# Optimization experiments

Hardware: AMD Instinct MI355X
Metric: run time of the kernel (lower is better)

## Reference

```python
import jax, jax.numpy as jnp
import numpy as np
from jax import lax

DIM = 384
NE = 8
TOPK = 2
HID = 4 * DIM
N, H, W = 32, 32, 32
EPS = 1e-6


def setup_inputs() -> dict:
    key = jax.random.key(0)
    ks = jax.random.split(key, 12)
    s = 0.02
    return {
        "input": jax.random.normal(ks[0], (N, DIM, H, W), dtype=jnp.float32),
        "dw_w": jax.random.normal(ks[1], (DIM, 1, 7, 7), dtype=jnp.float32) * s,
        "dw_b": jnp.zeros((DIM,), dtype=jnp.float32),
        "ln_g": jnp.ones((DIM,), dtype=jnp.float32),
        "ln_b": jnp.zeros((DIM,), dtype=jnp.float32),
        "gate_w": jax.random.normal(ks[2], (NE, DIM), dtype=jnp.float32) * s,
        "w1": jax.random.normal(ks[3], (NE, DIM, HID), dtype=jnp.float32) * s,
        "b1": jnp.zeros((NE, HID), dtype=jnp.float32),
        "w2": jax.random.normal(ks[4], (NE, HID, DIM), dtype=jnp.float32) * s,
        "b2": jnp.zeros((NE, DIM), dtype=jnp.float32),
        "layer_scale": jnp.ones((DIM, 1, 1), dtype=jnp.float32) * 1e-6,
    }


def reference(input, dw_w, dw_b, ln_g, ln_b, gate_w, w1, b1, w2, b2, layer_scale):
    # depthwise 7x7 conv, padding 3, groups=DIM  (NCHW)
    x = lax.conv_general_dilated(
        input, dw_w, window_strides=(1, 1), padding=((3, 3), (3, 3)),
        dimension_numbers=("NCHW", "OIHW", "NCHW"), feature_group_count=DIM,
    ) + dw_b[None, :, None, None]
    # permute to NHWC, layernorm over C with eps=1e-6
    x = jnp.transpose(x, (0, 2, 3, 1))
    mu = jnp.mean(x, axis=-1, keepdims=True)
    var = jnp.mean(jnp.square(x - mu), axis=-1, keepdims=True)
    x = (x - mu) * lax.rsqrt(var + EPS) * ln_g + ln_b

    x_flat = x.reshape(-1, DIM)  # [T, C]
    logits = x_flat @ gate_w.T   # [T, NE]
    topv, topi = lax.top_k(logits, TOPK)
    weights = jax.nn.softmax(topv, axis=-1)  # [T, K]

    # combine: out[t] = sum_e gate_e[t] * Expert_e(x_flat[t]), gate nonzero only for top-k
    out = jnp.zeros_like(x_flat)
    for e in range(NE):
        we = jnp.sum(jnp.where(topi == e, weights, 0.0), axis=-1)  # [T]
        h = jax.nn.gelu(x_flat @ w1[e] + b1[e], approximate=False)
        y = h @ w2[e] + b2[e]
        out = out + y * we[:, None]

    out = out.reshape(N, H, W, DIM)
    out = jnp.transpose(out, (0, 3, 1, 2))  # back to NCHW
    out = layer_scale[None] * out           # [C,1,1] broadcast
    # stochastic_depth prob 0.0 -> identity
    return input + out
```

## Files before the change

kernel.cpp:

```cpp
#include <hip/hip_runtime.h>
#include <hip/hip_bf16.h>

typedef __attribute__((ext_vector_type(4))) float  f32x4;
typedef __attribute__((ext_vector_type(8))) short  s16x8;
typedef __attribute__((ext_vector_type(8))) unsigned short u16x8;
typedef __attribute__((ext_vector_type(4))) unsigned short u16x4;

#define DIM 384
#define NE 8
#define HID 1536
#define NB 32
#define HW 1024
#define T_TOK 32768

__device__ __forceinline__ unsigned short f2bf(float f) {
    unsigned int u = __float_as_uint(f);
    u = (u + 0x7fffu + ((u >> 16) & 1u)) >> 16;
    return (unsigned short)u;
}
__device__ __forceinline__ float bf2f(unsigned short u) {
    return __uint_as_float((unsigned int)u << 16);
}

__global__ __launch_bounds__(256) void k_transpose(const float* __restrict__ src,
                                                   unsigned short* __restrict__ dst,
                                                   int R, int C) {
    int b = blockIdx.x;
    int ctiles = C >> 5;
    int rtiles = R >> 5;
    int ct = b % ctiles;
    int rt = (b / ctiles) % rtiles;
    int e  = b / (ctiles * rtiles);
    __shared__ float t[32][33];
    int tid = threadIdx.x;
    const float* s = src + (size_t)e * R * C;
    unsigned short* d = dst + (size_t)e * C * R;
#pragma unroll
    for (int k = 0; k < 4; ++k) {
        int idx = k * 256 + tid;
        int rr = idx >> 5, cc = idx & 31;
        t[rr][cc] = s[(size_t)(rt * 32 + rr) * C + ct * 32 + cc];
    }
    __syncthreads();
#pragma unroll
    for (int k = 0; k < 4; ++k) {
        int idx = k * 256 + tid;
        int cc = idx >> 5, rr = idx & 31;
        d[(size_t)(ct * 32 + cc) * R + rt * 32 + rr] = f2bf(t[rr][cc]);
    }
}

__global__ __launch_bounds__(256) void k_conv(const float* __restrict__ in,
                                              const float* __restrict__ dw_w,
                                              const float* __restrict__ dw_b,
                                              float* __restrict__ xconv) {
    int nc = blockIdx.x;
    int c = nc % DIM;
    __shared__ float tile[38 * 38];
    __shared__ float wt[49];
    const float* plane = in + (size_t)nc * HW;
    int tid = threadIdx.x;
    if (tid < 49) wt[tid] = dw_w[c * 49 + tid];
    for (int idx = tid; idx < 38 * 38; idx += 256) {
        int ty = idx / 38, tx = idx % 38;
        int ih = ty - 3, iw = tx - 3;
        float v = 0.f;
        if ((unsigned)ih < 32u && (unsigned)iw < 32u) v = plane[ih * 32 + iw];
        tile[idx] = v;
    }
    __syncthreads();
    float bias = dw_b[c];
    int w = tid & 31, h0 = (tid >> 5) << 2;
    float acc[4] = {bias, bias, bias, bias};
#pragma unroll
    for (int iy = 0; iy < 10; ++iy) {
        float r[7];
#pragma unroll
        for (int dx = 0; dx < 7; ++dx) r[dx] = tile[(h0 + iy) * 38 + w + dx];
#pragma unroll
        for (int o = 0; o < 4; ++o) {
            int dy = iy - o;
            if (dy >= 0 && dy < 7) {
                float a = 0.f;
#pragma unroll
                for (int dx = 0; dx < 7; ++dx) a += r[dx] * wt[dy * 7 + dx];
                acc[o] += a;
            }
        }
    }
    float* outp = xconv + (size_t)nc * HW;
#pragma unroll
    for (int o = 0; o < 4; ++o) outp[(h0 + o) * 32 + w] = acc[o];
}

__global__ __launch_bounds__(256) void k_ln_gate(const float* __restrict__ xconv,
                                                 const float* __restrict__ ln_g,
                                                 const float* __restrict__ ln_b,
                                                 const float* __restrict__ gate_w,
                                                 unsigned short* __restrict__ lnout,
                                                 int* __restrict__ lists,
                                                 float* __restrict__ wgts,
                                                 int* __restrict__ counts) {
    __shared__ float xs[32][385];
    __shared__ float gw[8][384];
    __shared__ float gls[384], bls[384];
    __shared__ int hcnt[8], hbase[8];
    __shared__ int lexp[32][2];
    __shared__ int lpos[32][2];
    __shared__ float lw[32][2];

    int b = blockIdx.x;
    int n = b >> 5;
    int hw0 = (b & 31) << 5;
    int tid = threadIdx.x;

    for (int i = tid; i < 384; i += 256) { gls[i] = ln_g[i]; bls[i] = ln_b[i]; }
    for (int i = tid; i < 8 * 384; i += 256) gw[i / 384][i % 384] = gate_w[i];
    if (tid < 8) hcnt[tid] = 0;

    const float* base = xconv + (size_t)n * DIM * HW + hw0;
#pragma unroll
    for (int k = 0; k < 48; ++k) {
        int idx = k * 256 + tid;
        int c = idx >> 5, j = idx & 31;
        xs[j][c] = base[(size_t)c * HW + j];
    }
    __syncthreads();

    int tok = tid >> 3, jj = tid & 7;
    float sum = 0.f, sq = 0.f;
#pragma unroll
    for (int k = 0; k < 48; ++k) {
        float v = xs[tok][jj + 8 * k];
        sum += v; sq += v * v;
    }
#pragma unroll
    for (int m = 1; m < 8; m <<= 1) { sum += __shfl_xor(sum, m); sq += __shfl_xor(sq, m); }
    float mu = sum * (1.f / 384.f);
    float var = sq * (1.f / 384.f) - mu * mu;
    float rstd = rsqrtf(var + 1e-6f);

    int tglob = n * HW + hw0 + tok;
    float p[8] = {0, 0, 0, 0, 0, 0, 0, 0};
#pragma unroll
    for (int k = 0; k < 48; ++k) {
        int c = jj + 8 * k;
        float v = (xs[tok][c] - mu) * rstd * gls[c] + bls[c];
        lnout[(size_t)tglob * DIM + c] = f2bf(v);
#pragma unroll
        for (int e = 0; e < 8; ++e) p[e] += v * gw[e][c];
    }
#pragma unroll
    for (int e = 0; e < 8; ++e)
#pragma unroll
        for (int m = 1; m < 8; m <<= 1) p[e] += __shfl_xor(p[e], m);

    if (jj == 0) {
        int i0 = 0; float v0 = p[0];
#pragma unroll
        for (int e = 1; e < 8; ++e) if (p[e] > v0) { v0 = p[e]; i0 = e; }
        int i1 = -1; float v1 = -1e30f;
#pragma unroll
        for (int e = 0; e < 8; ++e) if (e != i0 && p[e] > v1) { v1 = p[e]; i1 = e; }
        float w0 = 1.f / (1.f + __expf(v1 - v0));
        float w1 = 1.f - w0;
        lexp[tok][0] = i0; lexp[tok][1] = i1;
        lw[tok][0] = w0;  lw[tok][1] = w1;
        lpos[tok][0] = atomicAdd(&hcnt[i0], 1);
        lpos[tok][1] = atomicAdd(&hcnt[i1], 1);
    }
    __syncthreads();
    if (tid < 8) hbase[tid] = atomicAdd(&counts[tid], hcnt[tid]);
    __syncthreads();
    if (jj == 0) {
#pragma unroll
        for (int s = 0; s < 2; ++s) {
            int e = lexp[tok][s];
            int pos = hbase[e] + lpos[tok][s];
            lists[e * T_TOK + pos] = (tglob << 1) | s;
            wgts[e * T_TOK + pos] = lw[tok][s];
        }
    }
}

__global__ __launch_bounds__(256, 2) void k_moe(const unsigned short* __restrict__ ln,
                                                const unsigned short* __restrict__ w1t,
                                                const unsigned short* __restrict__ w2t,
                                                const float* __restrict__ b1,
                                                const float* __restrict__ b2,
                                                const int* __restrict__ lists,
                                                const float* __restrict__ wgts,
                                                const int* __restrict__ counts,
                                                unsigned short* __restrict__ y0,
                                                unsigned short* __restrict__ y1) {
    int e    = blockIdx.x & 7;
    int tile = blockIdx.x >> 3;
    int cnt = counts[e];
    if (tile * 64 >= cnt) return;

    __shared__ unsigned short X[64][392];
    __shared__ unsigned short Hs[64][136];
    __shared__ int   ents[64];
    __shared__ float wrow[64];

    int tid = threadIdx.x;
    if (tid < 64) {
        int idx = tile * 64 + tid;
        if (idx < cnt) { ents[tid] = lists[e * T_TOK + idx]; wrow[tid] = wgts[e * T_TOK + idx]; }
        else           { ents[tid] = -1;                     wrow[tid] = 0.f; }
    }
    __syncthreads();

    {
        int row = tid >> 2, q = tid & 3;
        int ent = ents[row];
        int tok = (ent < 0) ? 0 : (ent >> 1);
        const u16x8* src = (const u16x8*)(ln + (size_t)tok * DIM);
        u16x8* dst = (u16x8*)(&X[row][0]);
#pragma unroll
        for (int r = 0; r < 12; ++r) dst[q + r * 4] = src[q + r * 4];
    }
    __syncthreads();

    int wid = tid >> 6;
    int lane = tid & 63;
    int lr = lane & 15;
    int lq = lane >> 4;

    const s16x8* q1 = (const s16x8*)(w1t + ((size_t)e * HID + wid * 32 + lr) * DIM + lq * 8);
    const s16x8* q2 = (const s16x8*)(w2t + ((size_t)e * DIM + wid * 96 + lr) * HID + lq * 8);

    f32x4 Yacc[4][6] = {};

    for (int hc = 0; hc < 12; ++hc) {
        const s16x8* q1h = q1 + hc * 6144;
        f32x4 bv0 = *(const f32x4*)&b1[e * HID + hc * 128 + wid * 32 + lq * 4];
        f32x4 bv1 = *(const f32x4*)&b1[e * HID + hc * 128 + wid * 32 + 16 + lq * 4];
        f32x4 Hf[4][2];
#pragma unroll
        for (int m = 0; m < 4; ++m) { Hf[m][0] = bv0; Hf[m][1] = bv1; }
        __builtin_amdgcn_s_setprio(1);
#pragma unroll
        for (int k = 0; k < 12; ++k) {
            s16x8 a0 = *(const s16x8*)&X[ 0 + lr][k * 32 + lq * 8];
            s16x8 a1 = *(const s16x8*)&X[16 + lr][k * 32 + lq * 8];
            s16x8 a2 = *(const s16x8*)&X[32 + lr][k * 32 + lq * 8];
            s16x8 a3 = *(const s16x8*)&X[48 + lr][k * 32 + lq * 8];
            s16x8 w0 = q1h[k * 4];
            s16x8 w1f = q1h[768 + k * 4];
            Hf[0][0] = __builtin_amdgcn_mfma_f32_16x16x32_bf16(w0, a0, Hf[0][0], 0, 0, 0);
            Hf[1][0] = __builtin_amdgcn_mfma_f32_16x16x32_bf16(w0, a1, Hf[1][0], 0, 0, 0);
            Hf[2][0] = __builtin_amdgcn_mfma_f32_16x16x32_bf16(w0, a2, Hf[2][0], 0, 0, 0);
            Hf[3][0] = __builtin_amdgcn_mfma_f32_16x16x32_bf16(w0, a3, Hf[3][0], 0, 0, 0);
            Hf[0][1] = __builtin_amdgcn_mfma_f32_16x16x32_bf16(w1f, a0, Hf[0][1], 0, 0, 0);
            Hf[1][1] = __builtin_amdgcn_mfma_f32_16x16x32_bf16(w1f, a1, Hf[1][1], 0, 0, 0);
            Hf[2][1] = __builtin_amdgcn_mfma_f32_16x16x32_bf16(w1f, a2, Hf[2][1], 0, 0, 0);
            Hf[3][1] = __builtin_amdgcn_mfma_f32_16x16x32_bf16(w1f, a3, Hf[3][1], 0, 0, 0);
        }
        __builtin_amdgcn_s_setprio(0);
#pragma unroll
        for (int nj = 0; nj < 2; ++nj) {
#pragma unroll
            for (int m = 0; m < 4; ++m) {
                u16x4 pk;
#pragma unroll
                for (int r = 0; r < 4; ++r) {
                    float v = Hf[m][nj][r];
                    float t = v * fmaf(v * v, -0.07135481627f, -1.5957691216f);
                    float g = v * __builtin_amdgcn_rcpf(1.f + __expf(t));
                    pk[r] = f2bf(g);
                }
                *(u16x4*)&Hs[m * 16 + lr][wid * 32 + nj * 16 + lq * 4] = pk;
            }
        }
        asm volatile("s_waitcnt lgkmcnt(0)" ::: "memory");
        __builtin_amdgcn_s_barrier();
        __builtin_amdgcn_sched_barrier(0);
        __builtin_amdgcn_s_setprio(1);
#pragma unroll
        for (int k2 = 0; k2 < 4; ++k2) {
            s16x8 a0 = *(const s16x8*)&Hs[ 0 + lr][k2 * 32 + lq * 8];
            s16x8 a1 = *(const s16x8*)&Hs[16 + lr][k2 * 32 + lq * 8];
            s16x8 a2 = *(const s16x8*)&Hs[32 + lr][k2 * 32 + lq * 8];
            s16x8 a3 = *(const s16x8*)&Hs[48 + lr][k2 * 32 + lq * 8];
#pragma unroll
            for (int nj = 0; nj < 6; ++nj) {
                s16x8 wfr = q2[nj * 3072 + hc * 16 + k2 * 4];
                Yacc[0][nj] = __builtin_amdgcn_mfma_f32_16x16x32_bf16(wfr, a0, Yacc[0][nj], 0, 0, 0);
                Yacc[1][nj] = __builtin_amdgcn_mfma_f32_16x16x32_bf16(wfr, a1, Yacc[1][nj], 0, 0, 0);
                Yacc[2][nj] = __builtin_amdgcn_mfma_f32_16x16x32_bf16(wfr, a2, Yacc[2][nj], 0, 0, 0);
                Yacc[3][nj] = __builtin_amdgcn_mfma_f32_16x16x32_bf16(wfr, a3, Yacc[3][nj], 0, 0, 0);
            }
        }
        __builtin_amdgcn_s_setprio(0);
        asm volatile("s_waitcnt lgkmcnt(0)" ::: "memory");
        __builtin_amdgcn_s_barrier();
        __builtin_amdgcn_sched_barrier(0);
    }

    f32x4 b2v[6];
#pragma unroll
    for (int nj = 0; nj < 6; ++nj)
        b2v[nj] = *(const f32x4*)&b2[e * DIM + wid * 96 + nj * 16 + lq * 4];
#pragma unroll
    for (int m = 0; m < 4; ++m) {
        int row = m * 16 + lr;
        int ent = ents[row];
        if (ent >= 0) {
            float wv = wrow[row];
            int tok = ent >> 1;
            unsigned short* yb = (ent & 1) ? y1 : y0;
#pragma unroll
            for (int nj = 0; nj < 6; ++nj) {
                u16x4 pk;
#pragma unroll
                for (int r = 0; r < 4; ++r)
                    pk[r] = f2bf((Yacc[m][nj][r] + b2v[nj][r]) * wv);
                *(u16x4*)(yb + (size_t)tok * DIM + wid * 96 + nj * 16 + lq * 4) = pk;
            }
        }
    }
}

__global__ __launch_bounds__(256) void k_final(const float* __restrict__ input,
                                               const float* __restrict__ ls,
                                               const unsigned short* __restrict__ y0,
                                               const unsigned short* __restrict__ y1,
                                               float* __restrict__ out) {
    int b = blockIdx.x;
    int ct = b % 12;
    int hwt = (b / 12) % 32;
    int n = b / (12 * 32);
    int c0 = ct * 32, hw0 = hwt * 32;
    __shared__ float t[32][33];
    int tid = threadIdx.x;
    int t0 = n * HW + hw0;
#pragma unroll
    for (int k = 0; k < 2; ++k) {
        int idx = k * 256 + tid;
        int tl = idx >> 4, pr = idx & 15;
        size_t o = (size_t)(t0 + tl) * DIM + c0 + pr * 2;
        unsigned int a = *(const unsigned int*)(y0 + o);
        unsigned int c = *(const unsigned int*)(y1 + o);
        t[tl][pr * 2]     = bf2f((unsigned short)a) + bf2f((unsigned short)c);
        t[tl][pr * 2 + 1] = bf2f((unsigned short)(a >> 16)) + bf2f((unsigned short)(c >> 16));
    }
    __syncthreads();
#pragma unroll
    for (int k = 0; k < 4; ++k) {
        int idx = k * 256 + tid;
        int cl = idx >> 5, j = idx & 31;
        size_t o = ((size_t)n * DIM + c0 + cl) * HW + hw0 + j;
        out[o] = input[o] + ls[c0 + cl] * t[j][cl];
    }
}

extern "C" void kernel_launch(void* const* d_in, const int* in_sizes, int n_in,
                              void* d_out, int out_size, void* d_ws, size_t ws_size,
                              hipStream_t stream) {
    const float* input  = (const float*)d_in[0];
    const float* dw_w   = (const float*)d_in[1];
    const float* dw_b   = (const float*)d_in[2];
    const float* ln_g   = (const float*)d_in[3];
    const float* ln_b   = (const float*)d_in[4];
    const float* gate_w = (const float*)d_in[5];
    const float* w1     = (const float*)d_in[6];
    const float* b1     = (const float*)d_in[7];
    const float* w2     = (const float*)d_in[8];
    const float* b2     = (const float*)d_in[9];
    const float* lscale = (const float*)d_in[10];

    const size_t SZ_PLANE = (size_t)NB * DIM * HW * 4;
    const size_t SZ_YBF   = (size_t)T_TOK * DIM * 2;
    char* ws = (char*)d_ws;
    float* xconv = (float*)(ws + 0);
    unsigned short* y0 = (unsigned short*)(ws + 0);
    unsigned short* y1 = (unsigned short*)(ws + SZ_YBF);
    unsigned short* lnb = (unsigned short*)(ws + SZ_PLANE);
    unsigned short* w1t = (unsigned short*)(ws + SZ_PLANE + 25165824);
    unsigned short* w2t = (unsigned short*)(ws + SZ_PLANE + 25165824 + 9437184);
    int*   lists  = (int*)(ws + SZ_PLANE + 25165824 + 2 * 9437184);
    float* wgt    = (float*)(ws + SZ_PLANE + 25165824 + 2 * 9437184 + 1048576);
    int*   counts = (int*)(ws + SZ_PLANE + 25165824 + 2 * 9437184 + 2 * 1048576);
    const size_t needed = SZ_PLANE + 25165824 + 2 * 9437184 + 2 * 1048576 + 256;
    if (ws_size < needed) return;

    hipMemsetAsync(counts, 0, 32, stream);
    k_transpose<<<8 * 12 * 48, 256, 0, stream>>>(w1, w1t, DIM, HID);
    k_transpose<<<8 * 48 * 12, 256, 0, stream>>>(w2, w2t, HID, DIM);
    k_conv<<<NB * DIM, 256, 0, stream>>>(input, dw_w, dw_b, xconv);
    k_ln_gate<<<T_TOK / 32, 256, 0, stream>>>(xconv, ln_g, ln_b, gate_w, lnb, lists, wgt, counts);
    k_moe<<<NE * 512, 256, 0, stream>>>(lnb, w1t, w2t, b1, b2, lists, wgt, counts, y0, y1);
    k_final<<<NB * 32 * 12, 256, 0, stream>>>(input, lscale, y0, y1, (float*)d_out);
}
```

Baseline: 498.9 us.

## Double MoE token tile to 128 rows with 8 waves and preloaded weight fragments

The expert MLP kernel now handles 128 tokens per block with 512 threads instead of 64 with 256. Each wave owns a narrower slice of the hidden and output columns. W1 and W2 fragments are preloaded into registers once per hidden chunk and reused across eight 16-row token sub-tiles, which halves weight traffic per token. Token rows are gathered with nontemporal loads. The larger shared-memory footprint (about 135KB) allows only one block per CU, and the preloaded register arrays may push register pressure toward spilling.

```diff
diff --git a/kernel.cpp b/kernel.cpp
--- a/kernel.cpp
+++ b/kernel.cpp
@@ -183,7 +183,7 @@
     }
 }
 
-__global__ __launch_bounds__(256, 2) void k_moe(const unsigned short* __restrict__ ln,
+__global__ __launch_bounds__(512, 2) void k_moe(const unsigned short* __restrict__ ln,
                                                 const unsigned short* __restrict__ w1t,
                                                 const unsigned short* __restrict__ w2t,
                                                 const float* __restrict__ b1,
@@ -196,16 +196,16 @@
     int e    = blockIdx.x & 7;
     int tile = blockIdx.x >> 3;
     int cnt = counts[e];
-    if (tile * 64 >= cnt) return;
-
-    __shared__ unsigned short X[64][392];
-    __shared__ unsigned short Hs[64][136];
-    __shared__ int   ents[64];
-    __shared__ float wrow[64];
-
-    int tid = threadIdx.x;
-    if (tid < 64) {
-        int idx = tile * 64 + tid;
+    if (tile * 128 >= cnt) return;
+
+    __shared__ unsigned short X[128][392];
+    __shared__ unsigned short Hs[128][136];
+    __shared__ int   ents[128];
+    __shared__ float wrow[128];
+
+    int tid = threadIdx.x;
+    if (tid < 128) {
+        int idx = tile * 128 + tid;
         if (idx < cnt) { ents[tid] = lists[e * T_TOK + idx]; wrow[tid] = wgts[e * T_TOK + idx]; }
         else           { ents[tid] = -1;                     wrow[tid] = 0.f; }
     }
@@ -218,7 +218,7 @@
         const u16x8* src = (const u16x8*)(ln + (size_t)tok * DIM);
         u16x8* dst = (u16x8*)(&X[row][0]);
 #pragma unroll
-        for (int r = 0; r < 12; ++r) dst[q + r * 4] = src[q + r * 4];
+        for (int r = 0; r < 12; ++r) dst[q + r * 4] = __builtin_nontemporal_load(&src[q + r * 4]);
     }
     __syncthreads();
 
@@ -227,51 +227,47 @@
     int lr = lane & 15;
     int lq = lane >> 4;
 
-    const s16x8* q1 = (const s16x8*)(w1t + ((size_t)e * HID + wid * 32 + lr) * DIM + lq * 8);
-    const s16x8* q2 = (const s16x8*)(w2t + ((size_t)e * DIM + wid * 96 + lr) * HID + lq * 8);
-
-    f32x4 Yacc[4][6] = {};
+    const s16x8* q1 = (const s16x8*)(w1t + ((size_t)e * HID + wid * 16 + lr) * DIM + lq * 8);
+    const s16x8* q2 = (const s16x8*)(w2t + ((size_t)e * DIM + wid * 48 + lr) * HID + lq * 8);
+
+    f32x4 Yacc[3][8] = {};
 
     for (int hc = 0; hc < 12; ++hc) {
         const s16x8* q1h = q1 + hc * 6144;
-        f32x4 bv0 = *(const f32x4*)&b1[e * HID + hc * 128 + wid * 32 + lq * 4];
-        f32x4 bv1 = *(const f32x4*)&b1[e * HID + hc * 128 + wid * 32 + 16 + lq * 4];
-        f32x4 Hf[4][2];
-#pragma unroll
-        for (int m = 0; m < 4; ++m) { Hf[m][0] = bv0; Hf[m][1] = bv1; }
+        s16x8 wall[12];
+#pragma unroll
+        for (int k = 0; k < 12; ++k) wall[k] = q1h[k * 4];
+        f32x4 bv = *(const f32x4*)&b1[e * HID + hc * 128 + wid * 16 + lq * 4];
+        f32x4 Hf[8];
+#pragma unroll
+        for (int m = 0; m < 8; ++m) Hf[m] = bv;
         __builtin_amdgcn_s_setprio(1);
 #pragma unroll
         for (int k = 0; k < 12; ++k) {
-            s16x8 a0 = *(const s16x8*)&X[ 0 + lr][k * 32 + lq * 8];
-            s16x8 a1 = *(const s16x8*)&X[16 + lr][k * 32 + lq * 8];
-            s16x8 a2 = *(const s16x8*)&X[32 + lr][k * 32 + lq * 8];
-            s16x8 a3 = *(const s16x8*)&X[48 + lr][k * 32 + lq * 8];
-            s16x8 w0 = q1h[k * 4];
-            s16x8 w1f = q1h[768 + k * 4];
-            Hf[0][0] = __builtin_amdgcn_mfma_f32_16x16x32_bf16(w0, a0, Hf[0][0], 0, 0, 0);
-            Hf[1][0] = __builtin_amdgcn_mfma_f32_16x16x32_bf16(w0, a1, Hf[1][0], 0, 0, 0);
-            Hf[2][0] = __builtin_amdgcn_mfma_f32_16x16x32_bf16(w0, a2, Hf[2][0], 0, 0, 0);
-            Hf[3][0] = __builtin_amdgcn_mfma_f32_16x16x32_bf16(w0, a3, Hf[3][0], 0, 0, 0);
-            Hf[0][1] = __builtin_amdgcn_mfma_f32_16x16x32_bf16(w1f, a0, Hf[0][1], 0, 0, 0);
-            Hf[1][1] = __builtin_amdgcn_mfma_f32_16x16x32_bf16(w1f, a1, Hf[1][1], 0, 0, 0);
-            Hf[2][1] = __builtin_amdgcn_mfma_f32_16x16x32_bf16(w1f, a2, Hf[2][1], 0, 0, 0);
-            Hf[3][1] = __builtin_amdgcn_mfma_f32_16x16x32_bf16(w1f, a3, Hf[3][1], 0, 0, 0);
+#pragma unroll
+            for (int m = 0; m < 8; ++m) {
+                s16x8 a = *(const s16x8*)&X[m * 16 + lr][k * 32 + lq * 8];
+                Hf[m] = __builtin_amdgcn_mfma_f32_16x16x32_bf16(wall[k], a, Hf[m], 0, 0, 0);
+            }
         }
         __builtin_amdgcn_s_setprio(0);
-#pragma unroll
-        for (int nj = 0; nj < 2; ++nj) {
-#pragma unroll
-            for (int m = 0; m < 4; ++m) {
-                u16x4 pk;
-#pragma unroll
-                for (int r = 0; r < 4; ++r) {
-                    float v = Hf[m][nj][r];
-                    float t = v * fmaf(v * v, -0.07135481627f, -1.5957691216f);
-                    float g = v * __builtin_amdgcn_rcpf(1.f + __expf(t));
-                    pk[r] = f2bf(g);
-                }
-                *(u16x4*)&Hs[m * 16 + lr][wid * 32 + nj * 16 + lq * 4] = pk;
-            }
+        s16x8 vall[12];
+#pragma unroll
+        for (int t = 0; t < 12; ++t) {
+            int nj = t % 3, k2 = t / 3;
+            vall[t] = q2[nj * 3072 + hc * 16 + k2 * 4];
+        }
+#pragma unroll
+        for (int m = 0; m < 8; ++m) {
+            u16x4 pk;
+#pragma unroll
+            for (int r = 0; r < 4; ++r) {
+                float v = Hf[m][r];
+                float t = v * fmaf(v * v, -0.07135481627f, -1.5957691216f);
+                float g = v * __builtin_amdgcn_rcpf(1.f + __expf(t));
+                pk[r] = f2bf(g);
+            }
+            *(u16x4*)&Hs[m * 16 + lr][wid * 16 + lq * 4] = pk;
         }
         asm volatile("s_waitcnt lgkmcnt(0)" ::: "memory");
         __builtin_amdgcn_s_barrier();
@@ -279,17 +275,13 @@
         __builtin_amdgcn_s_setprio(1);
 #pragma unroll
         for (int k2 = 0; k2 < 4; ++k2) {
-            s16x8 a0 = *(const s16x8*)&Hs[ 0 + lr][k2 * 32 + lq * 8];
-            s16x8 a1 = *(const s16x8*)&Hs[16 + lr][k2 * 32 + lq * 8];
-            s16x8 a2 = *(const s16x8*)&Hs[32 + lr][k2 * 32 + lq * 8];
-            s16x8 a3 = *(const s16x8*)&Hs[48 + lr][k2 * 32 + lq * 8];
-#pragma unroll
-            for (int nj = 0; nj < 6; ++nj) {
-                s16x8 wfr = q2[nj * 3072 + hc * 16 + k2 * 4];
-                Yacc[0][nj] = __builtin_amdgcn_mfma_f32_16x16x32_bf16(wfr, a0, Yacc[0][nj], 0, 0, 0);
-                Yacc[1][nj] = __builtin_amdgcn_mfma_f32_16x16x32_bf16(wfr, a1, Yacc[1][nj], 0, 0, 0);
-                Yacc[2][nj] = __builtin_amdgcn_mfma_f32_16x16x32_bf16(wfr, a2, Yacc[2][nj], 0, 0, 0);
-                Yacc[3][nj] = __builtin_amdgcn_mfma_f32_16x16x32_bf16(wfr, a3, Yacc[3][nj], 0, 0, 0);
+#pragma unroll
+            for (int m = 0; m < 8; ++m) {
+                s16x8 a = *(const s16x8*)&Hs[m * 16 + lr][k2 * 32 + lq * 8];
+#pragma unroll
+                for (int nj = 0; nj < 3; ++nj) {
+                    Yacc[nj][m] = __builtin_amdgcn_mfma_f32_16x16x32_bf16(vall[k2 * 3 + nj], a, Yacc[nj][m], 0, 0, 0);
+                }
             }
         }
         __builtin_amdgcn_s_setprio(0);
@@ -298,12 +290,12 @@
         __builtin_amdgcn_sched_barrier(0);
     }
 
-    f32x4 b2v[6];
-#pragma unroll
-    for (int nj = 0; nj < 6; ++nj)
-        b2v[nj] = *(const f32x4*)&b2[e * DIM + wid * 96 + nj * 16 + lq * 4];
-#pragma unroll
-    for (int m = 0; m < 4; ++m) {
+    f32x4 b2v[3];
+#pragma unroll
+    for (int nj = 0; nj < 3; ++nj)
+        b2v[nj] = *(const f32x4*)&b2[e * DIM + wid * 48 + nj * 16 + lq * 4];
+#pragma unroll
+    for (int m = 0; m < 8; ++m) {
         int row = m * 16 + lr;
         int ent = ents[row];
         if (ent >= 0) {
@@ -311,12 +303,12 @@
             int tok = ent >> 1;
             unsigned short* yb = (ent & 1) ? y1 : y0;
 #pragma unroll
-            for (int nj = 0; nj < 6; ++nj) {
+            for (int nj = 0; nj < 3; ++nj) {
                 u16x4 pk;
 #pragma unroll
                 for (int r = 0; r < 4; ++r)
-                    pk[r] = f2bf((Yacc[m][nj][r] + b2v[nj][r]) * wv);
-                *(u16x4*)(yb + (size_t)tok * DIM + wid * 96 + nj * 16 + lq * 4) = pk;
+                    pk[r] = f2bf((Yacc[nj][m][r] + b2v[nj][r]) * wv);
+                *(u16x4*)(yb + (size_t)tok * DIM + wid * 48 + nj * 16 + lq * 4) = pk;
             }
         }
     }
@@ -390,6 +382,6 @@
     k_transpose<<<8 * 48 * 12, 256, 0, stream>>>(w2, w2t, HID, DIM);
     k_conv<<<NB * DIM, 256, 0, stream>>>(input, dw_w, dw_b, xconv);
     k_ln_gate<<<T_TOK / 32, 256, 0, stream>>>(xconv, ln_g, ln_b, gate_w, lnb, lists, wgt, counts);
-    k_moe<<<NE * 512, 256, 0, stream>>>(lnb, w1t, w2t, b1, b2, lists, wgt, counts, y0, y1);
+    k_moe<<<NE * 256, 512, 0, stream>>>(lnb, w1t, w2t, b1, b2, lists, wgt, counts, y0, y1);
     k_final<<<NB * 32 * 12, 256, 0, stream>>>(input, lscale, y0, y1, (float*)d_out);
 }
```

Result: faster. 427.6 us (-14.3%).
